# Optimization experiments

Hardware: AMD Instinct MI355X
Metric: run time of the kernel (lower is better)

The kernel has to match this reference:

```python
import jax, jax.numpy as jnp
from jax import lax
import numpy as np

B, C, H, W = 32, 256, 56, 56
R = max(1, C // 16)  # reduced channels = 16
K = 7                # spatial kernel


def setup_inputs() -> dict:
    key = jax.random.key(0)
    k_x, k1, k2, k3 = jax.random.split(key, 4)
    x = jax.random.normal(k_x, (B, C, H, W), dtype=jnp.float32)
    # shared MLP 1x1 convs (bias=False): stored as 2D matrices
    w1 = jax.random.normal(k1, (R, C), dtype=jnp.float32) * (1.0 / np.sqrt(C))
    w2 = jax.random.normal(k2, (C, R), dtype=jnp.float32) * (1.0 / np.sqrt(R))
    # spatial 7x7 conv: 2 in-channels (avg,max) -> 1 out, OIHW
    w_sp = jax.random.normal(k3, (1, 2, K, K), dtype=jnp.float32) * (1.0 / np.sqrt(2 * K * K))
    return {"x": x, "w1": w1, "w2": w2, "w_sp": w_sp}


def reference(x, w1, w2, w_sp):
    # ---- Channel attention ----
    avg = jnp.mean(x, axis=(2, 3))            # (B, C)
    mx = jnp.max(x, axis=(2, 3))              # (B, C)

    def mlp(v):  # shared 1x1-conv MLP on pooled vectors
        return jnp.einsum('cr,br->bc', w2, jax.nn.relu(jnp.einsum('rc,bc->br', w1, v)))

    ca = jax.nn.sigmoid(mlp(avg) + mlp(mx))[:, :, None, None]  # (B, C, 1, 1)
    xc = x * ca                                # (B, C, H, W)

    # ---- Spatial attention ----
    pooled = jnp.stack([jnp.mean(xc, axis=1), jnp.max(xc, axis=1)], axis=1)  # (B, 2, H, W)
    pad = (K - 1) // 2
    sa = jax.nn.sigmoid(
        lax.conv_general_dilated(pooled, w_sp, window_strides=(1, 1),
                                 padding=[(pad, pad), (pad, pad)],
                                 dimension_numbers=('NCHW', 'OIHW', 'NCHW')))  # (B, 1, H, W)

    # ---- Residual ----
    return x + xc * sa
```

## Files before the change

### kernel.cpp

```cpp
#include <hip/hip_runtime.h>
#include <math.h>

#define B_ 32
#define C_ 256
#define H_ 56
#define W_ 56
#define HW_ (H_*W_)
#define Q_ (HW_/4)
#define R_ 16
#define K_ 7

typedef float nat_f4 __attribute__((ext_vector_type(4)));

__device__ __forceinline__ float sigmoidf_(float v) { return 1.0f / (1.0f + __expf(-v)); }

__device__ __forceinline__ void nt_store4(float4 v, float4* p) {
    nat_f4 nv;
    nv.x = v.x; nv.y = v.y; nv.z = v.z; nv.w = v.w;
    __builtin_nontemporal_store(nv, (nat_f4*)p);
}

__device__ __forceinline__ void mlp_ca_block(int b,
        const float* __restrict__ avg, const float* __restrict__ mxv,
        const float* __restrict__ w1, const float* __restrict__ w2,
        float* sA, float* sM, float* hh, float* sca) {
    const int t = threadIdx.x;
    sA[t] = avg[b * C_ + t];
    sM[t] = mxv[b * C_ + t];
    __syncthreads();
    const int r = t >> 4, seg = t & 15;
    float pa = 0.f, pm = 0.f;
    #pragma unroll
    for (int i = 0; i < 16; ++i) {
        const float wv = w1[r * C_ + seg * 16 + i];
        pa += wv * sA[seg * 16 + i];
        pm += wv * sM[seg * 16 + i];
    }
    #pragma unroll
    for (int off = 8; off >= 1; off >>= 1) {
        pa += __shfl_xor(pa, off, 64);
        pm += __shfl_xor(pm, off, 64);
    }
    if (seg == 0) hh[r] = fmaxf(pa, 0.f) + fmaxf(pm, 0.f);
    __syncthreads();
    float acc = 0.f;
    #pragma unroll
    for (int rr = 0; rr < R_; ++rr) acc += w2[t * R_ + rr] * hh[rr];
    sca[t] = sigmoidf_(acc);
    __syncthreads();
}

__global__ void __launch_bounds__(256)
k_pool(const float* __restrict__ x, float* __restrict__ avg,
       float* __restrict__ mxv) {
    const int tid  = threadIdx.x;
    const int lane = tid & 63;
    const int wave = tid >> 6;
    const int map  = (blockIdx.x << 2) + wave;

    const float4* xp = (const float4*)(x + (size_t)map * HW_);
    float s = 0.0f, m = -INFINITY;
    #pragma unroll
    for (int k = 0; k < 12; ++k) {
        float4 v = xp[(k << 6) + lane];
        s += v.x + v.y + v.z + v.w;
        m = fmaxf(m, fmaxf(fmaxf(v.x, v.y), fmaxf(v.z, v.w)));
    }
    if (lane < 16) {
        float4 v = xp[768 + lane];
        s += v.x + v.y + v.z + v.w;
        m = fmaxf(m, fmaxf(fmaxf(v.x, v.y), fmaxf(v.z, v.w)));
    }
    #pragma unroll
    for (int off = 32; off > 0; off >>= 1) {
        s += __shfl_xor(s, off, 64);
        m = fmaxf(m, __shfl_xor(m, off, 64));
    }
    if (lane == 0) {
        avg[map] = s * (1.0f / HW_);
        mxv[map] = m;
    }
}

__global__ void __launch_bounds__(256)
k_spatial_pool(const float* __restrict__ x, const float* __restrict__ avg,
               const float* __restrict__ mxv, const float* __restrict__ w1,
               const float* __restrict__ w2, float* __restrict__ pooled) {
    const int b  = blockIdx.y;
    const int q0 = blockIdx.x * 16;
    const int t  = threadIdx.x;
    const int tq = t & 15;
    const int tc = t >> 4;
    const int q  = q0 + tq;

    __shared__ float sA[C_], sM[C_], sca[C_], hh[R_];
    mlp_ca_block(b, avg, mxv, w1, w2, sA, sM, hh, sca);

    const float4* xp = (const float4*)(x + (size_t)b * C_ * HW_);

    float4 s = {0.f, 0.f, 0.f, 0.f};
    float4 m = {-INFINITY, -INFINITY, -INFINITY, -INFINITY};
    #pragma unroll 4
    for (int i = 0; i < 16; ++i) {
        const int c = tc * 16 + i;
        const float a = sca[c];
        float4 v = xp[(size_t)c * Q_ + q];
        v.x *= a; v.y *= a; v.z *= a; v.w *= a;
        s.x += v.x; s.y += v.y; s.z += v.z; s.w += v.w;
        m.x = fmaxf(m.x, v.x); m.y = fmaxf(m.y, v.y);
        m.z = fmaxf(m.z, v.z); m.w = fmaxf(m.w, v.w);
    }

    __shared__ float4 ls[256];
    __shared__ float4 lm[256];
    ls[t] = s; lm[t] = m;
    __syncthreads();
    #pragma unroll
    for (int st = 8; st >= 1; st >>= 1) {
        if (tc < st) {
            const int o = t + st * 16;
            float4 os = ls[o], om = lm[o];
            s.x += os.x; s.y += os.y; s.z += os.z; s.w += os.w;
            m.x = fmaxf(m.x, om.x); m.y = fmaxf(m.y, om.y);
            m.z = fmaxf(m.z, om.z); m.w = fmaxf(m.w, om.w);
            ls[t] = s; lm[t] = m;
        }
        __syncthreads();
    }
    if (tc == 0) {
        const float inv = 1.0f / C_;
        float4 sm4 = {s.x * inv, s.y * inv, s.z * inv, s.w * inv};
        ((float4*)(pooled + (size_t)b * 2 * HW_))[q]       = sm4;
        ((float4*)(pooled + (size_t)b * 2 * HW_ + HW_))[q] = m;
    }
}

__global__ void __launch_bounds__(256)
k_conv_finalize(const float* __restrict__ x, const float* __restrict__ pooled,
                const float* __restrict__ wsp, const float* __restrict__ avg,
                const float* __restrict__ mxv, const float* __restrict__ w1,
                const float* __restrict__ w2, float* __restrict__ out) {
    const int b   = blockIdx.y;
    const int r0  = blockIdx.x * 2;
    const int tid = threadIdx.x;

    __shared__ float PH[2][8][62];
    __shared__ __align__(16) float ssa[112];
    __shared__ float sA[C_], sM[C_], sca[C_], hh[R_];
    __shared__ float wc[2 * K_ * K_];

    if (tid < 2 * K_ * K_) wc[tid] = wsp[tid];
    mlp_ca_block(b, avg, mxv, w1, w2, sA, sM, hh, sca);

    for (int idx = tid; idx < 992; idx += 256) {
        const int plane = idx / 496;
        const int rem   = idx - plane * 496;
        const int lr    = rem / 62;
        const int cpad  = rem - lr * 62;
        const int row   = r0 - 3 + lr;
        const int col   = cpad - 3;
        float v = 0.0f;
        if (row >= 0 && row < H_ && col >= 0 && col < W_)
            v = pooled[((size_t)b * 2 + plane) * HW_ + row * W_ + col];
        PH[plane][lr][cpad] = v;
    }
    __syncthreads();

    if (tid < 112) {
        const int prow = tid / 56;
        const int pcol = tid - prow * 56;
        float acc = 0.0f;
        #pragma unroll
        for (int ky = 0; ky < K_; ++ky) {
            #pragma unroll
            for (int kx = 0; kx < K_; ++kx) {
                acc += wc[ky * K_ + kx]          * PH[0][prow + ky][pcol + kx]
                     + wc[49 + ky * K_ + kx]     * PH[1][prow + ky][pcol + kx];
            }
        }
        ssa[tid] = sigmoidf_(acc);
    }
    __syncthreads();

    const int cg   = tid >> 5;
    const int lane = tid & 31;
    if (lane < 28) {
        const float4* xb = (const float4*)(x + (size_t)b * C_ * HW_);
        float4* ob = (float4*)(out + (size_t)b * C_ * HW_);
        const int base = r0 * 14;
        const float4 s4 = ((const float4*)ssa)[lane];
        #pragma unroll 4
        for (int g = 0; g < 32; ++g) {
            const int c = (g << 3) + cg;
            const float a = sca[c];
            const size_t o = (size_t)c * Q_ + base + lane;
            float4 v = xb[o];
            float4 r;
            r.x = v.x * (1.0f + a * s4.x);
            r.y = v.y * (1.0f + a * s4.y);
            r.z = v.z * (1.0f + a * s4.z);
            r.w = v.w * (1.0f + a * s4.w);
            nt_store4(r, ob + o);
        }
    }
}

extern "C" void kernel_launch(void* const* d_in, const int* in_sizes, int n_in,
                              void* d_out, int out_size, void* d_ws, size_t ws_size,
                              hipStream_t stream) {
    const float* x   = (const float*)d_in[0];
    const float* w1  = (const float*)d_in[1];
    const float* w2  = (const float*)d_in[2];
    const float* wsp = (const float*)d_in[3];
    float* out = (float*)d_out;

    float* ws     = (float*)d_ws;
    float* avg    = ws;
    float* mx     = avg + B_ * C_;
    float* pooled = mx + B_ * C_;

    k_pool<<<(B_ * C_) / 4, 256, 0, stream>>>(x, avg, mx);

    {
        dim3 g(Q_ / 16, B_);
        k_spatial_pool<<<g, 256, 0, stream>>>(x, avg, mx, w1, w2, pooled);
    }

    {
        dim3 g(H_ / 2, B_);
        k_conv_finalize<<<g, 256, 0, stream>>>(x, pooled, wsp, avg, mx, w1, w2, out);
    }
}
```

Before: 224.7 us.

## Fuse channel pooling, spatial conv and finalize into one kernel with halo recompute

Merges the spatial channel-pooling kernel into the conv/finalize kernel. Each block handles 4 output rows and recomputes channel mean/max for a 10-row halo window directly from x, so the pooled intermediate buffer and one launch go away. The cost is redundant reads of x for the halo rows (about 2.5x the channel-pooling traffic for those rows). The grid also shrinks to 14x32 blocks, which may underfill the GPU.

```diff
diff --git a/kernel.cpp b/kernel.cpp
--- a/kernel.cpp
+++ b/kernel.cpp
@@ -83,124 +83,115 @@
 }
 
 __global__ void __launch_bounds__(256)
-k_spatial_pool(const float* __restrict__ x, const float* __restrict__ avg,
-               const float* __restrict__ mxv, const float* __restrict__ w1,
-               const float* __restrict__ w2, float* __restrict__ pooled) {
-    const int b  = blockIdx.y;
-    const int q0 = blockIdx.x * 16;
-    const int t  = threadIdx.x;
-    const int tq = t & 15;
-    const int tc = t >> 4;
-    const int q  = q0 + tq;
-
-    __shared__ float sA[C_], sM[C_], sca[C_], hh[R_];
+k_sa_finalize(const float* __restrict__ x, const float* __restrict__ wsp,
+              const float* __restrict__ avg, const float* __restrict__ mxv,
+              const float* __restrict__ w1, const float* __restrict__ w2,
+              float* __restrict__ out) {
+    const int b    = blockIdx.y;
+    const int r0   = blockIdx.x * 4;
+    const int tid  = threadIdx.x;
+    const int lane = tid & 63;
+    const int w    = tid >> 6;
+
+    __shared__ float  sA[C_], sM[C_], sca[C_], hh[R_];
+    __shared__ float4 ps[4][140];
+    __shared__ float4 pm[4][140];
+    __shared__ float  PH[2][10][62];
+    __shared__ __align__(16) float ssa[224];
+    __shared__ float  wc[2 * K_ * K_];
+
+    if (tid < 2 * K_ * K_) wc[tid] = wsp[tid];
     mlp_ca_block(b, avg, mxv, w1, w2, sA, sM, hh, sca);
 
-    const float4* xp = (const float4*)(x + (size_t)b * C_ * HW_);
-
-    float4 s = {0.f, 0.f, 0.f, 0.f};
-    float4 m = {-INFINITY, -INFINITY, -INFINITY, -INFINITY};
-    #pragma unroll 4
-    for (int i = 0; i < 16; ++i) {
-        const int c = tc * 16 + i;
-        const float a = sca[c];
-        float4 v = xp[(size_t)c * Q_ + q];
-        v.x *= a; v.y *= a; v.z *= a; v.w *= a;
-        s.x += v.x; s.y += v.y; s.z += v.z; s.w += v.w;
-        m.x = fmaxf(m.x, v.x); m.y = fmaxf(m.y, v.y);
-        m.z = fmaxf(m.z, v.z); m.w = fmaxf(m.w, v.w);
-    }
-
-    __shared__ float4 ls[256];
-    __shared__ float4 lm[256];
-    ls[t] = s; lm[t] = m;
-    __syncthreads();
-    #pragma unroll
-    for (int st = 8; st >= 1; st >>= 1) {
-        if (tc < st) {
-            const int o = t + st * 16;
-            float4 os = ls[o], om = lm[o];
+    if (tid < 120) {
+        const int plane = tid / 60, rem = tid % 60;
+        const int hr = rem / 6, k = rem % 6;
+        const int col = (k < 3) ? k : k + 56;
+        PH[plane][hr][col] = 0.f;
+    }
+
+    const float4* xb = (const float4*)(x + (size_t)b * C_ * HW_);
+    const int qoff = (r0 - 3) * 14;
+    #pragma unroll
+    for (int chunk = 0; chunk < 3; ++chunk) {
+        const int pf4 = chunk * 64 + lane;
+        if (pf4 < 140) {
+            const int q = pf4 + qoff;
+            float4 s = {0.f, 0.f, 0.f, 0.f};
+            float4 m = {0.f, 0.f, 0.f, 0.f};
+            if (q >= 0 && q < Q_) {
+                m.x = m.y = m.z = m.w = -INFINITY;
+                #pragma unroll 8
+                for (int i = 0; i < 64; ++i) {
+                    const int c = (w << 6) + i;
+                    const float a = sca[c];
+                    float4 v = xb[(size_t)c * Q_ + q];
+                    v.x *= a; v.y *= a; v.z *= a; v.w *= a;
+                    s.x += v.x; s.y += v.y; s.z += v.z; s.w += v.w;
+                    m.x = fmaxf(m.x, v.x); m.y = fmaxf(m.y, v.y);
+                    m.z = fmaxf(m.z, v.z); m.w = fmaxf(m.w, v.w);
+                }
+            }
+            ps[w][pf4] = s; pm[w][pf4] = m;
+        }
+    }
+    __syncthreads();
+
+    if (tid < 140) {
+        float4 s = ps[0][tid], m = pm[0][tid];
+        #pragma unroll
+        for (int k = 1; k < 4; ++k) {
+            float4 os = ps[k][tid], om = pm[k][tid];
             s.x += os.x; s.y += os.y; s.z += os.z; s.w += os.w;
             m.x = fmaxf(m.x, om.x); m.y = fmaxf(m.y, om.y);
             m.z = fmaxf(m.z, om.z); m.w = fmaxf(m.w, om.w);
-            ls[t] = s; lm[t] = m;
-        }
-        __syncthreads();
-    }
-    if (tc == 0) {
+        }
         const float inv = 1.0f / C_;
-        float4 sm4 = {s.x * inv, s.y * inv, s.z * inv, s.w * inv};
-        ((float4*)(pooled + (size_t)b * 2 * HW_))[q]       = sm4;
-        ((float4*)(pooled + (size_t)b * 2 * HW_ + HW_))[q] = m;
-    }
-}
-
-__global__ void __launch_bounds__(256)
-k_conv_finalize(const float* __restrict__ x, const float* __restrict__ pooled,
-                const float* __restrict__ wsp, const float* __restrict__ avg,
-                const float* __restrict__ mxv, const float* __restrict__ w1,
-                const float* __restrict__ w2, float* __restrict__ out) {
-    const int b   = blockIdx.y;
-    const int r0  = blockIdx.x * 2;
-    const int tid = threadIdx.x;
-
-    __shared__ float PH[2][8][62];
-    __shared__ __align__(16) float ssa[112];
-    __shared__ float sA[C_], sM[C_], sca[C_], hh[R_];
-    __shared__ float wc[2 * K_ * K_];
-
-    if (tid < 2 * K_ * K_) wc[tid] = wsp[tid];
-    mlp_ca_block(b, avg, mxv, w1, w2, sA, sM, hh, sca);
-
-    for (int idx = tid; idx < 992; idx += 256) {
-        const int plane = idx / 496;
-        const int rem   = idx - plane * 496;
-        const int lr    = rem / 62;
-        const int cpad  = rem - lr * 62;
-        const int row   = r0 - 3 + lr;
-        const int col   = cpad - 3;
-        float v = 0.0f;
-        if (row >= 0 && row < H_ && col >= 0 && col < W_)
-            v = pooled[((size_t)b * 2 + plane) * HW_ + row * W_ + col];
-        PH[plane][lr][cpad] = v;
-    }
-    __syncthreads();
-
-    if (tid < 112) {
-        const int prow = tid / 56;
-        const int pcol = tid - prow * 56;
+        const int hr = tid / 14, c4 = tid - hr * 14;
+        float* pa = &PH[0][hr][3 + c4 * 4];
+        float* pb = &PH[1][hr][3 + c4 * 4];
+        pa[0] = s.x * inv; pa[1] = s.y * inv; pa[2] = s.z * inv; pa[3] = s.w * inv;
+        pb[0] = m.x;       pb[1] = m.y;       pb[2] = m.z;       pb[3] = m.w;
+    }
+    __syncthreads();
+
+    if (tid < 224) {
+        const int orow = tid / 56, ocol = tid - orow * 56;
         float acc = 0.0f;
         #pragma unroll
         for (int ky = 0; ky < K_; ++ky) {
             #pragma unroll
             for (int kx = 0; kx < K_; ++kx) {
-                acc += wc[ky * K_ + kx]          * PH[0][prow + ky][pcol + kx]
-                     + wc[49 + ky * K_ + kx]     * PH[1][prow + ky][pcol + kx];
+                acc += wc[ky * K_ + kx]      * PH[0][orow + ky][ocol + kx]
+                     + wc[49 + ky * K_ + kx] * PH[1][orow + ky][ocol + kx];
             }
         }
         ssa[tid] = sigmoidf_(acc);
     }
     __syncthreads();
 
-    const int cg   = tid >> 5;
-    const int lane = tid & 31;
-    if (lane < 28) {
-        const float4* xb = (const float4*)(x + (size_t)b * C_ * HW_);
+    const int cg = tid >> 5;
+    const int ln = tid & 31;
+    if (ln < 28) {
         float4* ob = (float4*)(out + (size_t)b * C_ * HW_);
-        const int base = r0 * 14;
-        const float4 s4 = ((const float4*)ssa)[lane];
-        #pragma unroll 4
-        for (int g = 0; g < 32; ++g) {
-            const int c = (g << 3) + cg;
-            const float a = sca[c];
-            const size_t o = (size_t)c * Q_ + base + lane;
-            float4 v = xb[o];
-            float4 r;
-            r.x = v.x * (1.0f + a * s4.x);
-            r.y = v.y * (1.0f + a * s4.y);
-            r.z = v.z * (1.0f + a * s4.z);
-            r.w = v.w * (1.0f + a * s4.w);
-            nt_store4(r, ob + o);
+        #pragma unroll
+        for (int half = 0; half < 2; ++half) {
+            const int pos = half * 28 + ln;
+            const float4 s4 = ((const float4*)ssa)[pos];
+            const size_t base = (size_t)r0 * 14 + pos;
+            #pragma unroll 4
+            for (int g = 0; g < 32; ++g) {
+                const int c = (g << 3) + cg;
+                const float a = sca[c];
+                const size_t o = (size_t)c * Q_ + base;
+                float4 v = xb[o];
+                float4 r;
+                r.x = v.x * (1.0f + a * s4.x);
+                r.y = v.y * (1.0f + a * s4.y);
+                r.z = v.z * (1.0f + a * s4.z);
+                r.w = v.w * (1.0f + a * s4.w);
+                nt_store4(r, ob + o);
+            }
         }
     }
 }
@@ -214,20 +205,14 @@
     const float* wsp = (const float*)d_in[3];
     float* out = (float*)d_out;
 
-    float* ws     = (float*)d_ws;
-    float* avg    = ws;
-    float* mx     = avg + B_ * C_;
-    float* pooled = mx + B_ * C_;
+    float* ws  = (float*)d_ws;
+    float* avg = ws;
+    float* mx  = avg + B_ * C_;
 
     k_pool<<<(B_ * C_) / 4, 256, 0, stream>>>(x, avg, mx);
 
     {
-        dim3 g(Q_ / 16, B_);
-        k_spatial_pool<<<g, 256, 0, stream>>>(x, avg, mx, w1, w2, pooled);
-    }
-
-    {
-        dim3 g(H_ / 2, B_);
-        k_conv_finalize<<<g, 256, 0, stream>>>(x, pooled, wsp, avg, mx, w1, w2, out);
-    }
-}
+        dim3 g(H_ / 4, B_);
+        k_sa_finalize<<<g, 256, 0, stream>>>(x, wsp, avg, mx, w1, w2, out);
+    }
+}
```

New measurement: 240.4 us. 1.07x slower.
